# Performance work log

Measured on AMD Instinct MI355X. Metric: run time of the kernel, lower is better.

## Reference

```python
import jax, jax.numpy as jnp
import numpy as np

B, S, H = 2, 512, 768
E, M, R, R2 = 64, 64, 128, 128
NER_C, REL_C, SIZE_E, CLS = 10, 8, 32, 101
NEG = -1e30


def _linear(x, w, b):
    # torch nn.Linear convention: w is [out, in]
    return x @ w.T + b


def _span_pool(emb, masks):
    # emb [B,S,H], masks [B,K,S] -> masked max over tokens -> [B,K,H]
    neg = jnp.where(masks[..., None] != 0, 0.0, NEG)  # [B,K,S,1]
    return jnp.max(neg + emb[:, None, :, :], axis=2)


def _classify_spans(input_ids, emb, masks, size_emb, rep_w, rep_b, head_w, head_b):
    pool = _span_pool(emb, masks)                      # [B,K,H]
    cls_idx = jnp.argmax((input_ids == CLS).astype(jnp.int32), axis=1)
    ctx = emb[jnp.arange(emb.shape[0]), cls_idx]       # [B,H] (get_token)
    rep = jnp.concatenate([jnp.broadcast_to(ctx[:, None, :], pool.shape), pool, size_emb], axis=-1)
    clf = _linear(jax.nn.relu(_linear(rep, rep_w, rep_b)), head_w, head_b)
    return clf, pool


def _classify_relations(pool, size_emb, rels, rel_masks, emb, w1, b1, w2, b2, w3, b3):
    Bc = pool.shape[0]
    bidx = jnp.arange(Bc)[:, None, None]
    pairs = pool[bidx, rels].reshape(Bc, rels.shape[1], -1)        # [B,R,2H]
    size_pairs = size_emb[bidx, rels].reshape(Bc, rels.shape[1], -1)  # [B,R,2*SIZE_E]
    # masked max over context tokens (rel mask)
    ctx = jnp.max(jnp.where(rel_masks[..., None] != 0, 0.0, NEG) + emb[:, None, :, :], axis=2)
    ctx = jnp.where(jnp.any(rel_masks != 0, axis=-1)[..., None], ctx, 0.0)
    rel_repr = jnp.concatenate([ctx, pairs, size_pairs], axis=-1)  # [B,R,3H+2*SIZE_E]
    h = jax.nn.relu(_linear(rel_repr, w1, b1))
    h = jax.nn.relu(_linear(h, w2, b2))
    return _linear(h, w3, b3)


def setup_inputs():
    key = jax.random.key(0)
    ks = jax.random.split(key, 24)
    p = lambda k, shape: jax.random.normal(k, shape, jnp.float32) * 0.02
    ids = jax.random.randint(ks[0], (B, S), 2000, 30000)
    ids = ids.at[:, 0].set(CLS)  # exactly one cls token per row
    return dict(
        input_ids=ids,
        entity_masks=jax.random.randint(ks[1], (B, E, S), 0, 2).astype(jnp.int32),
        entity_sizes=jax.random.randint(ks[2], (B, E), 0, 100),
        mention_masks=jax.random.randint(ks[3], (B, M, S), 0, 2).astype(jnp.int32),
        mention_sizes=jax.random.randint(ks[4], (B, M), 0, 100),
        relations=jax.random.randint(ks[5], (B, R, 2), 0, E),
        rel_masks=jax.random.randint(ks[6], (B, R, S), 0, 2).astype(jnp.int32),
        references=jax.random.randint(ks[7], (B, R2, 2), 0, M),
        references_masks=jax.random.randint(ks[8], (B, R2, S), 0, 2).astype(jnp.int32),
        token_embedding=jax.random.normal(ks[9], (B, S, H), jnp.float32),
        ner_size_emb=p(ks[10], (100, SIZE_E)),
        emd_size_emb=p(ks[11], (100, SIZE_E)),
        ner_rep_w=p(ks[12], (H, 2 * H + SIZE_E)), ner_rep_b=jnp.zeros(H, jnp.float32),
        ner_head_w=p(ks[13], (NER_C, H)), ner_head_b=jnp.zeros(NER_C, jnp.float32),
        emd_rep_w=p(ks[14], (H, 2 * H + SIZE_E)), emd_rep_b=jnp.zeros(H, jnp.float32),
        emd_head_w=p(ks[15], (2, H)), emd_head_b=jnp.zeros(2, jnp.float32),
        rel_w1=p(ks[16], (H, 3 * H + 2 * SIZE_E)), rel_b1=jnp.zeros(H, jnp.float32),
        rel_w2=p(ks[17], (H, H)), rel_b2=jnp.zeros(H, jnp.float32),
        rel_w3=p(ks[18], (REL_C, H)), rel_b3=jnp.zeros(REL_C, jnp.float32),
        cr_w1=p(ks[19], (H, 3 * H + 2 * SIZE_E)), cr_b1=jnp.zeros(H, jnp.float32),
        cr_w2=p(ks[20], (H, H)), cr_b2=jnp.zeros(H, jnp.float32),
        cr_w3=p(ks[21], (1, H)), cr_b3=jnp.zeros(1, jnp.float32),
    )


def reference(input_ids, entity_masks, entity_sizes, mention_masks, mention_sizes,
              relations, rel_masks, references, references_masks, token_embedding,
              ner_size_emb, emd_size_emb,
              ner_rep_w, ner_rep_b, ner_head_w, ner_head_b,
              emd_rep_w, emd_rep_b, emd_head_w, emd_head_b,
              rel_w1, rel_b1, rel_w2, rel_b2, rel_w3, rel_b3,
              cr_w1, cr_b1, cr_w2, cr_b2, cr_w3, cr_b3):
    sz = ner_size_emb[entity_sizes]                                    # [B,E,SIZE_E]
    entity_clf, entity_pool = _classify_spans(input_ids, token_embedding, entity_masks, sz,
                                              ner_rep_w, ner_rep_b, ner_head_w, ner_head_b)
    rel_clf = _classify_relations(entity_pool, sz, relations, rel_masks, token_embedding,
                                  rel_w1, rel_b1, rel_w2, rel_b2, rel_w3, rel_b3)
    msz = emd_size_emb[mention_sizes]
    mention_clf, mention_pool = _classify_spans(input_ids, token_embedding, mention_masks, msz,
                                                emd_rep_w, emd_rep_b, emd_head_w, emd_head_b)
    ref_clf = _classify_relations(mention_pool, msz, references, references_masks, token_embedding,
                                  cr_w1, cr_b1, cr_w2, cr_b2, cr_w3, cr_b3)
    return entity_clf, rel_clf, mention_clf, ref_clf
```

## Files before the change

### kernel.cpp

```cpp
#include <hip/hip_runtime.h>
#include <hip/hip_bf16.h>

typedef __hip_bfloat16 bf16;
typedef __attribute__((ext_vector_type(8))) short short8;
typedef __attribute__((ext_vector_type(4))) float f32x4;

#define SS 512
#define HD 768
#define NEGC (-1e30f)
#define NSPLIT 8
#define TOK 64
#define POOL_BLOCKS 768
#define NCONV 128
#define D1_BLOCKS (POOL_BLOCKS + 4 + NCONV)

__device__ __forceinline__ short8 cvt8(float4 a, float4 b)
{
  union { bf16 h[8]; short8 s; } u;
  u.h[0] = __hip_bfloat16(a.x); u.h[1] = __hip_bfloat16(a.y);
  u.h[2] = __hip_bfloat16(a.z); u.h[3] = __hip_bfloat16(a.w);
  u.h[4] = __hip_bfloat16(b.x); u.h[5] = __hip_bfloat16(b.y);
  u.h[6] = __hip_bfloat16(b.z); u.h[7] = __hip_bfloat16(b.w);
  return u.s;
}

struct WC { const float* s; bf16* d; int n8; };
struct WC6 { WC c[6]; };

__global__ __launch_bounds__(256) void k_d1(
    const int* __restrict__ e_masks, const int* __restrict__ m_masks,
    const int* __restrict__ r_masks, const int* __restrict__ c_masks,
    const float* __restrict__ emb, const int* __restrict__ input_ids,
    const int* __restrict__ esizes, const int* __restrict__ msizes,
    const float* __restrict__ nsemb, const float* __restrict__ esemb,
    bf16* __restrict__ part, int* __restrict__ flags,
    bf16* __restrict__ sze, bf16* __restrict__ szm,
    bf16* __restrict__ ctxb, float* __restrict__ out, WC6 wc)
{
  int bx = blockIdx.x;
  int t  = threadIdx.x;

  if (bx >= POOL_BLOCKS) {
    int q = bx - POOL_BLOCKS;
    if (q == 0) {
      for (int i = t; i < 128 * 32; i += 256)
        sze[i] = __hip_bfloat16(nsemb[(size_t)esizes[i >> 5] * 32 + (i & 31)]);
    } else if (q == 1) {
      for (int i = t; i < 128 * 32; i += 256)
        szm[i] = __hip_bfloat16(esemb[(size_t)msizes[i >> 5] * 32 + (i & 31)]);
    } else if (q == 2) {
      __shared__ int s_cls;
      for (int b2 = 0; b2 < 2; b2++) {
        if (t == 0) s_cls = SS;
        __syncthreads();
        for (int s = t; s < SS; s += 256)
          if (input_ids[b2 * SS + s] == 101) atomicMin(&s_cls, s);
        __syncthreads();
        int ci = (s_cls == SS) ? 0 : s_cls;
        for (int hh = t; hh < HD; hh += 256)
          ctxb[(size_t)b2 * HD + hh] = __hip_bfloat16(emb[((size_t)b2 * SS + ci) * HD + hh]);
        __syncthreads();
      }
    } else if (q == 3) {
      for (int i = t; i < 3840; i += 256) out[i] = 0.f;
    } else {
      int cid = q - 4;
      #pragma unroll
      for (int seg = 0; seg < 6; seg++) {
        const float* s = wc.c[seg].s;
        bf16* dp = wc.c[seg].d;
        int n8 = wc.c[seg].n8;
        for (int i = cid * 256 + t; i < n8; i += NCONV * 256) {
          float4 f0 = *(const float4*)(s + (size_t)i * 8);
          float4 f1 = *(const float4*)(s + (size_t)i * 8 + 4);
          *(short8*)(dp + (size_t)i * 8) = cvt8(f0, f1);
        }
      }
    }
    return;
  }

  int g  = bx % 48;
  int b  = (bx / 48) & 1;
  int sp = bx / 96;
  int j0 = g * 8;

  const int* marr; int row0;
  if      (j0 < 64)  { marr = e_masks; row0 = b*64  +  j0;        }
  else if (j0 < 128) { marr = m_masks; row0 = b*64  + (j0-64);    }
  else if (j0 < 256) { marr = r_masks; row0 = b*128 + (j0-128);   }
  else               { marr = c_masks; row0 = b*128 + (j0-256);   }

  __shared__ unsigned s_pack[TOK];
  __shared__ unsigned s_any;
  if (t == 0) s_any = 0u;
  __syncthreads();

  int sbase = sp * TOK;
  if (t < TOK) {
    unsigned w = 0;
    #pragma unroll
    for (int k = 0; k < 8; k++) {
      int mm = marr[(size_t)(row0 + k) * SS + sbase + t];
      w |= (mm != 0 ? 1u : 0u) << k;
    }
    s_pack[t] = w;
    atomicOr(&s_any, w);
  }
  __syncthreads();

  float a0[8], a1[8], a2[8];
  #pragma unroll
  for (int k = 0; k < 8; k++) { a0[k] = -INFINITY; a1[k] = -INFINITY; a2[k] = -INFINITY; }

  const float* ep = emb + ((size_t)b * SS + sbase) * HD + t * 3;
  #pragma unroll 2
  for (int s = 0; s < TOK; s += 2) {
    float u0 = ep[0];
    float u1 = ep[1];
    float u2 = ep[2];
    float v0 = ep[HD];
    float v1 = ep[HD + 1];
    float v2 = ep[HD + 2];
    ep += 2 * HD;
    unsigned w0 = (unsigned)__builtin_amdgcn_readfirstlane((int)s_pack[s]);
    unsigned w1 = (unsigned)__builtin_amdgcn_readfirstlane((int)s_pack[s + 1]);
    #pragma unroll
    for (int k = 0; k < 8; k++) {
      float add0 = (w0 & (1u << k)) ? 0.f : NEGC;
      float add1 = (w1 & (1u << k)) ? 0.f : NEGC;
      a0[k] = fmaxf(fmaxf(a0[k], u0 + add0), v0 + add1);
      a1[k] = fmaxf(fmaxf(a1[k], u1 + add0), v1 + add1);
      a2[k] = fmaxf(fmaxf(a2[k], u2 + add0), v2 + add1);
    }
  }

  #pragma unroll
  for (int k = 0; k < 8; k++) {
    int sg = b * 384 + j0 + k;
    bf16* dst = part + ((size_t)sg * NSPLIT + sp) * HD + t * 3;
    dst[0] = __hip_bfloat16(a0[k]);
    dst[1] = __hip_bfloat16(a1[k]);
    dst[2] = __hip_bfloat16(a2[k]);
  }
  if (t < 8) flags[(size_t)(b * 384 + j0 + t) * NSPLIT + sp] = (int)((s_any >> t) & 1u);
}

__global__ __launch_bounds__(256) void k_combine(
    const bf16* __restrict__ part, const int* __restrict__ flags,
    bf16* __restrict__ epool, bf16* __restrict__ mpool,
    bf16* __restrict__ rctx, bf16* __restrict__ cctx)
{
  int sg = blockIdx.x;
  int b = sg / 384, j = sg % 384;
  int any = 0;
  #pragma unroll
  for (int sp = 0; sp < NSPLIT; sp++) any |= flags[(size_t)sg * NSPLIT + sp];

  int h = threadIdx.x * 3;
  float v0 = -INFINITY, v1 = -INFINITY, v2 = -INFINITY;
  #pragma unroll
  for (int sp = 0; sp < NSPLIT; sp++) {
    const bf16* src = part + ((size_t)sg * NSPLIT + sp) * HD + h;
    v0 = fmaxf(v0, (float)src[0]);
    v1 = fmaxf(v1, (float)src[1]);
    v2 = fmaxf(v2, (float)src[2]);
  }
  bf16* dst;
  if      (j < 64)  { dst = epool + ((size_t)b*64  + j)       * HD + h; }
  else if (j < 128) { dst = mpool + ((size_t)b*64  + (j-64))  * HD + h; }
  else if (j < 256) { dst = rctx  + ((size_t)b*128 + (j-128)) * HD + h;
                      if (!any) { v0 = 0.f; v1 = 0.f; v2 = 0.f; } }
  else              { dst = cctx  + ((size_t)b*128 + (j-256)) * HD + h;
                      if (!any) { v0 = 0.f; v1 = 0.f; v2 = 0.f; } }
  dst[0] = __hip_bfloat16(v0);
  dst[1] = __hip_bfloat16(v1);
  dst[2] = __hip_bfloat16(v2);
}

struct P1 {
  const bf16 *ctx, *pool, *sz; const int* ridx;
  const bf16* W; const float* bias;
  bf16* C;
  const float *hw, *hb; float* outp;
  int is_rel, N, K, Mtiles;
};
struct P1x4 { P1 p[4]; };

__global__ __launch_bounds__(256, 2) void k_gemm1(P1x4 args)
{
  int id = blockIdx.x;
  int x = id / 96;
  int r96 = id % 96;
  int y = r96 % 24, z = r96 / 24;
  P1 g = args.p[z];
  if (x >= g.Mtiles) return;
  int mt = x * 32, nt = y * 32;
  int wave = threadIdx.x >> 6, lane = threadIdx.x & 63;
  int lm = lane & 15, quad = lane >> 4;
  int K_ = g.K;

  const bf16 *g0[2], *g1[2], *g2[2], *g3[2], *g4[2];
  int rr[2] = { mt + lm, mt + 16 + lm };
  #pragma unroll
  for (int i = 0; i < 2; i++) {
    int rI = rr[i];
    if (g.is_rel) {
      int b = rI >> 7;
      int i0 = g.ridx[2 * rI], i1 = g.ridx[2 * rI + 1];
      g0[i] = g.ctx  + (size_t)rI * HD;
      g1[i] = g.pool + (size_t)(b * 64 + i0) * HD;
      g2[i] = g.pool + (size_t)(b * 64 + i1) * HD;
      g3[i] = g.sz   + (size_t)(b * 64 + i0) * 32;
      g4[i] = g.sz   + (size_t)(b * 64 + i1) * 32;
    } else {
      g0[i] = g.ctx  + (size_t)(rI >> 6) * HD;
      g1[i] = g.pool + (size_t)rI * HD;
      g2[i] = g.sz   + (size_t)rI * 32;
      g3[i] = g2[i]; g4[i] = g2[i];
    }
  }
  const bf16* w0p = g.W + (size_t)(nt + lm)      * K_ + quad * 8;
  const bf16* w1p = g.W + (size_t)(nt + 16 + lm) * K_ + quad * 8;

  f32x4 acc00 = {0.f,0.f,0.f,0.f}, acc01 = {0.f,0.f,0.f,0.f};
  f32x4 acc10 = {0.f,0.f,0.f,0.f}, acc11 = {0.f,0.f,0.f,0.f};

  for (int k32 = wave * 32; k32 < K_; k32 += 128) {
    const bf16 *b0, *b1;
    if      (k32 < 768)  { b0 = g0[0] + k32;          b1 = g0[1] + k32;          }
    else if (k32 < 1536) { b0 = g1[0] + (k32 - 768);  b1 = g1[1] + (k32 - 768);  }
    else if (k32 < 2304) { b0 = g2[0] + (k32 - 1536); b1 = g2[1] + (k32 - 1536); }
    else if (k32 < 2336) { b0 = g3[0] + (k32 - 2304); b1 = g3[1] + (k32 - 2304); }
    else                 { b0 = g4[0] + (k32 - 2336); b1 = g4[1] + (k32 - 2336); }
    short8 a0 = *(const short8*)((const short*)b0 + quad * 8);
    short8 a1 = *(const short8*)((const short*)b1 + quad * 8);
    short8 w0 = *(const short8*)(w0p + k32);
    short8 w1 = *(const short8*)(w1p + k32);
    acc00 = __builtin_amdgcn_mfma_f32_16x16x32_bf16(a0, w0, acc00, 0, 0, 0);
    acc01 = __builtin_amdgcn_mfma_f32_16x16x32_bf16(a0, w1, acc01, 0, 0, 0);
    acc10 = __builtin_amdgcn_mfma_f32_16x16x32_bf16(a1, w0, acc10, 0, 0, 0);
    acc11 = __builtin_amdgcn_mfma_f32_16x16x32_bf16(a1, w1, acc11, 0, 0, 0);
  }

  __shared__ float smem[4 * 32 * 32];
  #pragma unroll
  for (int reg = 0; reg < 4; reg++) {
    int rI = quad * 4 + reg;
    smem[wave*1024 + rI*32 + lm]             = acc00[reg];
    smem[wave*1024 + rI*32 + 16 + lm]        = acc01[reg];
    smem[wave*1024 + (16 + rI)*32 + lm]      = acc10[reg];
    smem[wave*1024 + (16 + rI)*32 + 16 + lm] = acc11[reg];
  }
  __syncthreads();

  int c = threadIdx.x & 31;
  int rb = threadIdx.x >> 5;
  float bb = g.bias[nt + c];
  #pragma unroll
  for (int i = 0; i < 4; i++) {
    int rI = rb + 8 * i;
    float v = smem[rI*32 + c] + smem[1024 + rI*32 + c] + smem[2048 + rI*32 + c] + smem[3072 + rI*32 + c];
    v = fmaxf(v + bb, 0.f);
    if (g.C) g.C[(size_t)(mt + rI) * HD + nt + c] = __hip_bfloat16(v);
    else     smem[rI*32 + c] = v;
  }
  __syncthreads();

  if (!g.C) {
    int rI = threadIdx.x >> 3, oi = threadIdx.x & 7;
    for (int o = oi; o < g.N; o += 8) {
      float s = 0.f;
      #pragma unroll
      for (int cc = 0; cc < 32; cc++) {
        int c2 = (cc + rI) & 31;
        s += smem[rI*32 + c2] * g.hw[(size_t)o * HD + nt + c2];
      }
      if (blockIdx.x % 96 < 24) ;
      if (y == 0) s += g.hb[o];
      atomicAdd(g.outp + (size_t)(mt + rI) * g.N + o, s);
    }
  }
}

struct P2 { const short* A; const bf16* W; const float* bias;
            const float *hw, *hb; float* outp; int N; };
struct P2x2 { P2 p[2]; };

__global__ __launch_bounds__(256, 2) void k_gemm2(P2x2 args)
{
  int id = blockIdx.x;
  int x = id / 48;
  int r48 = id % 48;
  int y = r48 % 24, z = r48 / 24;
  P2 g = args.p[z];
  int mt = x * 32, nt = y * 32;
  int wave = threadIdx.x >> 6, lane = threadIdx.x & 63;
  int lm = lane & 15, quad = lane >> 4;

  const short* a0p = g.A + (size_t)(mt + lm)      * HD + quad * 8;
  const short* a1p = g.A + (size_t)(mt + 16 + lm) * HD + quad * 8;
  const bf16* w0p = g.W + (size_t)(nt + lm)      * HD + quad * 8;
  const bf16* w1p = g.W + (size_t)(nt + 16 + lm) * HD + quad * 8;

  f32x4 acc00 = {0.f,0.f,0.f,0.f}, acc01 = {0.f,0.f,0.f,0.f};
  f32x4 acc10 = {0.f,0.f,0.f,0.f}, acc11 = {0.f,0.f,0.f,0.f};

  for (int k32 = wave * 32; k32 < HD; k32 += 128) {
    short8 a0 = *(const short8*)(a0p + k32);
    short8 a1 = *(const short8*)(a1p + k32);
    short8 w0 = *(const short8*)(w0p + k32);
    short8 w1 = *(const short8*)(w1p + k32);
    acc00 = __builtin_amdgcn_mfma_f32_16x16x32_bf16(a0, w0, acc00, 0, 0, 0);
    acc01 = __builtin_amdgcn_mfma_f32_16x16x32_bf16(a0, w1, acc01, 0, 0, 0);
    acc10 = __builtin_amdgcn_mfma_f32_16x16x32_bf16(a1, w0, acc10, 0, 0, 0);
    acc11 = __builtin_amdgcn_mfma_f32_16x16x32_bf16(a1, w1, acc11, 0, 0, 0);
  }

  __shared__ float smem[4 * 32 * 32];
  #pragma unroll
  for (int reg = 0; reg < 4; reg++) {
    int rI = quad * 4 + reg;
    smem[wave*1024 + rI*32 + lm]             = acc00[reg];
    smem[wave*1024 + rI*32 + 16 + lm]        = acc01[reg];
    smem[wave*1024 + (16 + rI)*32 + lm]      = acc10[reg];
    smem[wave*1024 + (16 + rI)*32 + 16 + lm] = acc11[reg];
  }
  __syncthreads();

  int c = threadIdx.x & 31;
  int rb = threadIdx.x >> 5;
  float bb = g.bias[nt + c];
  #pragma unroll
  for (int i = 0; i < 4; i++) {
    int rI = rb + 8 * i;
    float v = smem[rI*32 + c] + smem[1024 + rI*32 + c] + smem[2048 + rI*32 + c] + smem[3072 + rI*32 + c];
    smem[rI*32 + c] = fmaxf(v + bb, 0.f);
  }
  __syncthreads();

  int rI = threadIdx.x >> 3, oi = threadIdx.x & 7;
  for (int o = oi; o < g.N; o += 8) {
    float s = 0.f;
    #pragma unroll
    for (int cc = 0; cc < 32; cc++) {
      int c2 = (cc + rI) & 31;
      s += smem[rI*32 + c2] * g.hw[(size_t)o * HD + nt + c2];
    }
    if (y == 0) s += g.hb[o];
    atomicAdd(g.outp + (size_t)(mt + rI) * g.N + o, s);
  }
}

extern "C" void kernel_launch(void* const* d_in, const int* in_sizes, int n_in,
                              void* d_out, int out_size, void* d_ws, size_t ws_size,
                              hipStream_t stream)
{
  const int*   input_ids  = (const int*)d_in[0];
  const int*   e_masks    = (const int*)d_in[1];
  const int*   e_sizes    = (const int*)d_in[2];
  const int*   m_masks    = (const int*)d_in[3];
  const int*   m_sizes    = (const int*)d_in[4];
  const int*   relations  = (const int*)d_in[5];
  const int*   r_masks    = (const int*)d_in[6];
  const int*   references = (const int*)d_in[7];
  const int*   c_masks    = (const int*)d_in[8];
  const float* emb        = (const float*)d_in[9];
  const float* nsemb      = (const float*)d_in[10];
  const float* esemb      = (const float*)d_in[11];
  const float* ner_rep_w  = (const float*)d_in[12];
  const float* ner_rep_b  = (const float*)d_in[13];
  const float* ner_head_w = (const float*)d_in[14];
  const float* ner_head_b = (const float*)d_in[15];
  const float* emd_rep_w  = (const float*)d_in[16];
  const float* emd_rep_b  = (const float*)d_in[17];
  const float* emd_head_w = (const float*)d_in[18];
  const float* emd_head_b = (const float*)d_in[19];
  const float* rel_w1 = (const float*)d_in[20];
  const float* rel_b1 = (const float*)d_in[21];
  const float* rel_w2 = (const float*)d_in[22];
  const float* rel_b2 = (const float*)d_in[23];
  const float* rel_w3 = (const float*)d_in[24];
  const float* rel_b3 = (const float*)d_in[25];
  const float* cr_w1 = (const float*)d_in[26];
  const float* cr_b1 = (const float*)d_in[27];
  const float* cr_w2 = (const float*)d_in[28];
  const float* cr_b2 = (const float*)d_in[29];
  const float* cr_w3 = (const float*)d_in[30];
  const float* cr_b3 = (const float*)d_in[31];
  float* out = (float*)d_out;

  bf16* wsb = (bf16*)d_ws;
  size_t ob = 0;
  bf16* PART  = wsb + ob; ob += (size_t)NSPLIT * 768 * HD;
  bf16* EPOOL = wsb + ob; ob += (size_t)128 * HD;
  bf16* MPOOL = wsb + ob; ob += (size_t)128 * HD;
  bf16* RCTX  = wsb + ob; ob += (size_t)256 * HD;
  bf16* CCTX  = wsb + ob; ob += (size_t)256 * HD;
  bf16* SZE   = wsb + ob; ob += (size_t)128 * 32;
  bf16* SZM   = wsb + ob; ob += (size_t)128 * 32;
  bf16* CTXB  = wsb + ob; ob += (size_t)2 * HD;
  bf16* RH1   = wsb + ob; ob += (size_t)256 * HD;
  bf16* CH1   = wsb + ob; ob += (size_t)256 * HD;
  int*  FLAGS = (int*)(wsb + ob); ob += (size_t)2 * NSPLIT * 768;
  bf16* WB_NER = wsb + ob; ob += (size_t)HD * 1568;
  bf16* WB_EMD = wsb + ob; ob += (size_t)HD * 1568;
  bf16* WB_RW1 = wsb + ob; ob += (size_t)HD * 2368;
  bf16* WB_CW1 = wsb + ob; ob += (size_t)HD * 2368;
  bf16* WB_RW2 = wsb + ob; ob += (size_t)HD * HD;
  bf16* WB_CW2 = wsb + ob; ob += (size_t)HD * HD;

  WC6 wc;
  wc.c[0] = { ner_rep_w, WB_NER, HD * 1568 / 8 };
  wc.c[1] = { emd_rep_w, WB_EMD, HD * 1568 / 8 };
  wc.c[2] = { rel_w1,    WB_RW1, HD * 2368 / 8 };
  wc.c[3] = { cr_w1,     WB_CW1, HD * 2368 / 8 };
  wc.c[4] = { rel_w2,    WB_RW2, HD * HD / 8 };
  wc.c[5] = { cr_w2,     WB_CW2, HD * HD / 8 };

  k_d1<<<D1_BLOCKS, 256, 0, stream>>>(
      e_masks, m_masks, r_masks, c_masks, emb, input_ids,
      e_sizes, m_sizes, nsemb, esemb,
      PART, FLAGS, SZE, SZM, CTXB, out, wc);

  k_combine<<<768, 256, 0, stream>>>(PART, FLAGS, EPOOL, MPOOL, RCTX, CCTX);

  P1x4 a1;
  a1.p[0] = { CTXB, EPOOL, SZE, nullptr,    WB_NER, ner_rep_b,
              nullptr, ner_head_w, ner_head_b, out,        0, 10, 1568, 4 };
  a1.p[1] = { CTXB, MPOOL, SZM, nullptr,    WB_EMD, emd_rep_b,
              nullptr, emd_head_w, emd_head_b, out + 3328, 0, 2,  1568, 4 };
  a1.p[2] = { RCTX, EPOOL, SZE, relations,  WB_RW1, rel_b1,
              RH1, nullptr, nullptr, nullptr,              1, 0,  2368, 8 };
  a1.p[3] = { CCTX, MPOOL, SZM, references, WB_CW1, cr_b1,
              CH1, nullptr, nullptr, nullptr,              1, 0,  2368, 8 };
  k_gemm1<<<8 * 96, 256, 0, stream>>>(a1);

  P2x2 a2;
  a2.p[0] = { (const short*)RH1, WB_RW2, rel_b2, rel_w3, rel_b3, out + 1280, 8 };
  a2.p[1] = { (const short*)CH1, WB_CW2, cr_b2,  cr_w3,  cr_b3,  out + 3584, 1 };
  k_gemm2<<<8 * 48, 256, 0, stream>>>(a2);
}
```

Measured before the change: 190.7 us.

## Pool 16 spans per block, prefetch GEMM operands, compact GEMM grids

The pooling kernel now processes 16 spans per block instead of 8, halving the block count so each embedding load is reused across more masks. The cost is 48 accumulator registers per thread. Both GEMM kernels gain software prefetching of the next K-slice operands, so global loads overlap the MFMA work. The gemm1 grid is remapped to launch only the valid tiles, removing the early-exit blocks, and gemm2's block decomposition is reordered.

Measured after the change: 201.0 us. 5.4% more time.

```diff
diff --git a/kernel.cpp b/kernel.cpp
--- a/kernel.cpp
+++ b/kernel.cpp
@@ -10,7 +10,8 @@
 #define NEGC (-1e30f)
 #define NSPLIT 8
 #define TOK 64
-#define POOL_BLOCKS 768
+#define NSPAN 16
+#define POOL_BLOCKS 384
 #define NCONV 128
 #define D1_BLOCKS (POOL_BLOCKS + 4 + NCONV)
 
@@ -80,10 +81,10 @@
     return;
   }
 
-  int g  = bx % 48;
-  int b  = (bx / 48) & 1;
-  int sp = bx / 96;
-  int j0 = g * 8;
+  int g  = bx % 24;
+  int b  = (bx / 24) & 1;
+  int sp = bx / 48;
+  int j0 = g * NSPAN;
 
   const int* marr; int row0;
   if      (j0 < 64)  { marr = e_masks; row0 = b*64  +  j0;        }
@@ -100,7 +101,7 @@
   if (t < TOK) {
     unsigned w = 0;
     #pragma unroll
-    for (int k = 0; k < 8; k++) {
+    for (int k = 0; k < NSPAN; k++) {
       int mm = marr[(size_t)(row0 + k) * SS + sbase + t];
       w |= (mm != 0 ? 1u : 0u) << k;
     }
@@ -109,12 +110,11 @@
   }
   __syncthreads();
 
-  float a0[8], a1[8], a2[8];
-  #pragma unroll
-  for (int k = 0; k < 8; k++) { a0[k] = -INFINITY; a1[k] = -INFINITY; a2[k] = -INFINITY; }
+  float a0[NSPAN], a1[NSPAN], a2[NSPAN];
+  #pragma unroll
+  for (int k = 0; k < NSPAN; k++) { a0[k] = -INFINITY; a1[k] = -INFINITY; a2[k] = -INFINITY; }
 
   const float* ep = emb + ((size_t)b * SS + sbase) * HD + t * 3;
-  #pragma unroll 2
   for (int s = 0; s < TOK; s += 2) {
     float u0 = ep[0];
     float u1 = ep[1];
@@ -126,7 +126,7 @@
     unsigned w0 = (unsigned)__builtin_amdgcn_readfirstlane((int)s_pack[s]);
     unsigned w1 = (unsigned)__builtin_amdgcn_readfirstlane((int)s_pack[s + 1]);
     #pragma unroll
-    for (int k = 0; k < 8; k++) {
+    for (int k = 0; k < NSPAN; k++) {
       float add0 = (w0 & (1u << k)) ? 0.f : NEGC;
       float add1 = (w1 & (1u << k)) ? 0.f : NEGC;
       a0[k] = fmaxf(fmaxf(a0[k], u0 + add0), v0 + add1);
@@ -136,14 +136,14 @@
   }
 
   #pragma unroll
-  for (int k = 0; k < 8; k++) {
+  for (int k = 0; k < NSPAN; k++) {
     int sg = b * 384 + j0 + k;
     bf16* dst = part + ((size_t)sg * NSPLIT + sp) * HD + t * 3;
     dst[0] = __hip_bfloat16(a0[k]);
     dst[1] = __hip_bfloat16(a1[k]);
     dst[2] = __hip_bfloat16(a2[k]);
   }
-  if (t < 8) flags[(size_t)(b * 384 + j0 + t) * NSPLIT + sp] = (int)((s_any >> t) & 1u);
+  if (t < NSPAN) flags[(size_t)(b * 384 + j0 + t) * NSPLIT + sp] = (int)((s_any >> t) & 1u);
 }
 
 __global__ __launch_bounds__(256) void k_combine(
@@ -190,11 +190,13 @@
 __global__ __launch_bounds__(256, 2) void k_gemm1(P1x4 args)
 {
   int id = blockIdx.x;
-  int x = id / 96;
-  int r96 = id % 96;
-  int y = r96 % 24, z = r96 / 24;
+  int z, rem;
+  if      (id < 96)  { z = 0; rem = id;       }
+  else if (id < 192) { z = 1; rem = id - 96;  }
+  else if (id < 384) { z = 2; rem = id - 192; }
+  else               { z = 3; rem = id - 384; }
+  int x = rem / 24, y = rem % 24;
   P1 g = args.p[z];
-  if (x >= g.Mtiles) return;
   int mt = x * 32, nt = y * 32;
   int wave = threadIdx.x >> 6, lane = threadIdx.x & 63;
   int lm = lane & 15, quad = lane >> 4;
@@ -226,22 +228,37 @@
   f32x4 acc00 = {0.f,0.f,0.f,0.f}, acc01 = {0.f,0.f,0.f,0.f};
   f32x4 acc10 = {0.f,0.f,0.f,0.f}, acc11 = {0.f,0.f,0.f,0.f};
 
-  for (int k32 = wave * 32; k32 < K_; k32 += 128) {
+  auto ldA = [&](int k32, short8& a0, short8& a1) {
     const bf16 *b0, *b1;
     if      (k32 < 768)  { b0 = g0[0] + k32;          b1 = g0[1] + k32;          }
     else if (k32 < 1536) { b0 = g1[0] + (k32 - 768);  b1 = g1[1] + (k32 - 768);  }
     else if (k32 < 2304) { b0 = g2[0] + (k32 - 1536); b1 = g2[1] + (k32 - 1536); }
     else if (k32 < 2336) { b0 = g3[0] + (k32 - 2304); b1 = g3[1] + (k32 - 2304); }
     else                 { b0 = g4[0] + (k32 - 2336); b1 = g4[1] + (k32 - 2336); }
-    short8 a0 = *(const short8*)((const short*)b0 + quad * 8);
-    short8 a1 = *(const short8*)((const short*)b1 + quad * 8);
-    short8 w0 = *(const short8*)(w0p + k32);
-    short8 w1 = *(const short8*)(w1p + k32);
+    a0 = *(const short8*)((const short*)b0 + quad * 8);
+    a1 = *(const short8*)((const short*)b1 + quad * 8);
+  };
+
+  int k32 = wave * 32;
+  short8 a0, a1, w0, w1;
+  ldA(k32, a0, a1);
+  w0 = *(const short8*)(w0p + k32);
+  w1 = *(const short8*)(w1p + k32);
+  for (int kn = k32 + 128; kn < K_; kn += 128) {
+    short8 na0, na1, nw0, nw1;
+    ldA(kn, na0, na1);
+    nw0 = *(const short8*)(w0p + kn);
+    nw1 = *(const short8*)(w1p + kn);
     acc00 = __builtin_amdgcn_mfma_f32_16x16x32_bf16(a0, w0, acc00, 0, 0, 0);
     acc01 = __builtin_amdgcn_mfma_f32_16x16x32_bf16(a0, w1, acc01, 0, 0, 0);
     acc10 = __builtin_amdgcn_mfma_f32_16x16x32_bf16(a1, w0, acc10, 0, 0, 0);
     acc11 = __builtin_amdgcn_mfma_f32_16x16x32_bf16(a1, w1, acc11, 0, 0, 0);
-  }
+    a0 = na0; a1 = na1; w0 = nw0; w1 = nw1;
+  }
+  acc00 = __builtin_amdgcn_mfma_f32_16x16x32_bf16(a0, w0, acc00, 0, 0, 0);
+  acc01 = __builtin_amdgcn_mfma_f32_16x16x32_bf16(a0, w1, acc01, 0, 0, 0);
+  acc10 = __builtin_amdgcn_mfma_f32_16x16x32_bf16(a1, w0, acc10, 0, 0, 0);
+  acc11 = __builtin_amdgcn_mfma_f32_16x16x32_bf16(a1, w1, acc11, 0, 0, 0);
 
   __shared__ float smem[4 * 32 * 32];
   #pragma unroll
@@ -276,7 +293,6 @@
         int c2 = (cc + rI) & 31;
         s += smem[rI*32 + c2] * g.hw[(size_t)o * HD + nt + c2];
       }
-      if (blockIdx.x % 96 < 24) ;
       if (y == 0) s += g.hb[o];
       atomicAdd(g.outp + (size_t)(mt + rI) * g.N + o, s);
     }
@@ -290,9 +306,9 @@
 __global__ __launch_bounds__(256, 2) void k_gemm2(P2x2 args)
 {
   int id = blockIdx.x;
-  int x = id / 48;
-  int r48 = id % 48;
-  int y = r48 % 24, z = r48 / 24;
+  int z = id / 192;
+  int rem = id % 192;
+  int x = rem / 24, y = rem % 24;
   P2 g = args.p[z];
   int mt = x * 32, nt = y * 32;
   int wave = threadIdx.x >> 6, lane = threadIdx.x & 63;
@@ -306,16 +322,26 @@
   f32x4 acc00 = {0.f,0.f,0.f,0.f}, acc01 = {0.f,0.f,0.f,0.f};
   f32x4 acc10 = {0.f,0.f,0.f,0.f}, acc11 = {0.f,0.f,0.f,0.f};
 
-  for (int k32 = wave * 32; k32 < HD; k32 += 128) {
-    short8 a0 = *(const short8*)(a0p + k32);
-    short8 a1 = *(const short8*)(a1p + k32);
-    short8 w0 = *(const short8*)(w0p + k32);
-    short8 w1 = *(const short8*)(w1p + k32);
+  int k32 = wave * 32;
+  short8 a0 = *(const short8*)(a0p + k32);
+  short8 a1 = *(const short8*)(a1p + k32);
+  short8 w0 = *(const short8*)(w0p + k32);
+  short8 w1 = *(const short8*)(w1p + k32);
+  for (int kn = k32 + 128; kn < HD; kn += 128) {
+    short8 na0 = *(const short8*)(a0p + kn);
+    short8 na1 = *(const short8*)(a1p + kn);
+    short8 nw0 = *(const short8*)(w0p + kn);
+    short8 nw1 = *(const short8*)(w1p + kn);
     acc00 = __builtin_amdgcn_mfma_f32_16x16x32_bf16(a0, w0, acc00, 0, 0, 0);
     acc01 = __builtin_amdgcn_mfma_f32_16x16x32_bf16(a0, w1, acc01, 0, 0, 0);
     acc10 = __builtin_amdgcn_mfma_f32_16x16x32_bf16(a1, w0, acc10, 0, 0, 0);
     acc11 = __builtin_amdgcn_mfma_f32_16x16x32_bf16(a1, w1, acc11, 0, 0, 0);
-  }
+    a0 = na0; a1 = na1; w0 = nw0; w1 = nw1;
+  }
+  acc00 = __builtin_amdgcn_mfma_f32_16x16x32_bf16(a0, w0, acc00, 0, 0, 0);
+  acc01 = __builtin_amdgcn_mfma_f32_16x16x32_bf16(a0, w1, acc01, 0, 0, 0);
+  acc10 = __builtin_amdgcn_mfma_f32_16x16x32_bf16(a1, w0, acc10, 0, 0, 0);
+  acc11 = __builtin_amdgcn_mfma_f32_16x16x32_bf16(a1, w1, acc11, 0, 0, 0);
 
   __shared__ float smem[4 * 32 * 32];
   #pragma unroll
@@ -434,10 +460,10 @@
               RH1, nullptr, nullptr, nullptr,              1, 0,  2368, 8 };
   a1.p[3] = { CCTX, MPOOL, SZM, references, WB_CW1, cr_b1,
               CH1, nullptr, nullptr, nullptr,              1, 0,  2368, 8 };
-  k_gemm1<<<8 * 96, 256, 0, stream>>>(a1);
+  k_gemm1<<<576, 256, 0, stream>>>(a1);
 
   P2x2 a2;
   a2.p[0] = { (const short*)RH1, WB_RW2, rel_b2, rel_w3, rel_b3, out + 1280, 8 };
   a2.p[1] = { (const short*)CH1, WB_CW2, cr_b2,  cr_w3,  cr_b3,  out + 3584, 1 };
-  k_gemm2<<<8 * 48, 256, 0, stream>>>(a2);
-}
+  k_gemm2<<<384, 256, 0, stream>>>(a2);
+}
```

## Pre-tile bf16 weights and hidden activations into MFMA fragment layout

Applied to the files above, without the earlier changes.

The fp32-to-bf16 weight conversion now writes the weights in a 16-row by 32-column fragment-blocked layout, so each MFMA operand load in the GEMMs reads a contiguous 512-element tile instead of striding across rows. The first GEMM writes its hidden output in the same tiled layout for the second GEMM to consume. Conversion work is split into per-16-row units over more blocks. The first GEMM grid is compacted so it no longer launches idle blocks for the entity and mention tasks. This trades a more complex index mapping in conversion and epilogue for better-coalesced weight and activation reads.

Measured after the change: 187.2 us. Within noise of the previous version (-1.8%).

```diff
diff --git a/kernel.cpp b/kernel.cpp
--- a/kernel.cpp
+++ b/kernel.cpp
@@ -11,7 +11,7 @@
 #define NSPLIT 8
 #define TOK 64
 #define POOL_BLOCKS 768
-#define NCONV 128
+#define NCONV 252
 #define D1_BLOCKS (POOL_BLOCKS + 4 + NCONV)
 
 __device__ __forceinline__ short8 cvt8(float4 a, float4 b)
@@ -24,7 +24,7 @@
   return u.s;
 }
 
-struct WC { const float* s; bf16* d; int n8; };
+struct WC { const float* s; bf16* d; int K; };
 struct WC6 { WC c[6]; };
 
 __global__ __launch_bounds__(256) void k_d1(
@@ -65,15 +65,23 @@
       for (int i = t; i < 3840; i += 256) out[i] = 0.f;
     } else {
       int cid = q - 4;
-      #pragma unroll
-      for (int seg = 0; seg < 6; seg++) {
+      for (int u = cid; u < 288; u += NCONV) {
+        int seg = u / 48, nblk = u % 48;
         const float* s = wc.c[seg].s;
         bf16* dp = wc.c[seg].d;
-        int n8 = wc.c[seg].n8;
-        for (int i = cid * 256 + t; i < n8; i += NCONV * 256) {
-          float4 f0 = *(const float4*)(s + (size_t)i * 8);
-          float4 f1 = *(const float4*)(s + (size_t)i * 8 + 4);
-          *(short8*)(dp + (size_t)i * 8) = cvt8(f0, f1);
+        int K = wc.c[seg].K;
+        int KB = K >> 5;
+        int nchunk = K * 2;
+        const float* srow = s + (size_t)nblk * 16 * K;
+        bf16* drow = dp + (size_t)nblk * KB * 512;
+        for (int c8 = t; c8 < nchunk; c8 += 256) {
+          int kblk = c8 >> 6;
+          int lm   = (c8 >> 2) & 15;
+          int quad = c8 & 3;
+          const float* sp = srow + (size_t)lm * K + kblk * 32 + quad * 8;
+          float4 f0 = *(const float4*)sp;
+          float4 f1 = *(const float4*)(sp + 4);
+          *(short8*)(drow + (size_t)kblk * 512 + lm * 32 + quad * 8) = cvt8(f0, f1);
         }
       }
     }
@@ -190,15 +198,18 @@
 __global__ __launch_bounds__(256, 2) void k_gemm1(P1x4 args)
 {
   int id = blockIdx.x;
-  int x = id / 96;
-  int r96 = id % 96;
-  int y = r96 % 24, z = r96 / 24;
+  int z, rem;
+  if      (id < 96)  { z = 0; rem = id;       }
+  else if (id < 192) { z = 1; rem = id - 96;  }
+  else if (id < 384) { z = 2; rem = id - 192; }
+  else               { z = 3; rem = id - 384; }
+  int x = rem / 24, y = rem % 24;
   P1 g = args.p[z];
-  if (x >= g.Mtiles) return;
   int mt = x * 32, nt = y * 32;
   int wave = threadIdx.x >> 6, lane = threadIdx.x & 63;
   int lm = lane & 15, quad = lane >> 4;
   int K_ = g.K;
+  int KB = K_ >> 5;
 
   const bf16 *g0[2], *g1[2], *g2[2], *g3[2], *g4[2];
   int rr[2] = { mt + lm, mt + 16 + lm };
@@ -220,8 +231,8 @@
       g3[i] = g2[i]; g4[i] = g2[i];
     }
   }
-  const bf16* w0p = g.W + (size_t)(nt + lm)      * K_ + quad * 8;
-  const bf16* w1p = g.W + (size_t)(nt + 16 + lm) * K_ + quad * 8;
+  const bf16* w0p = g.W + (size_t)(nt >> 4) * KB * 512 + lm * 32 + quad * 8;
+  const bf16* w1p = w0p + (size_t)KB * 512;
 
   f32x4 acc00 = {0.f,0.f,0.f,0.f}, acc01 = {0.f,0.f,0.f,0.f};
   f32x4 acc10 = {0.f,0.f,0.f,0.f}, acc11 = {0.f,0.f,0.f,0.f};
@@ -235,8 +246,8 @@
     else                 { b0 = g4[0] + (k32 - 2336); b1 = g4[1] + (k32 - 2336); }
     short8 a0 = *(const short8*)((const short*)b0 + quad * 8);
     short8 a1 = *(const short8*)((const short*)b1 + quad * 8);
-    short8 w0 = *(const short8*)(w0p + k32);
-    short8 w1 = *(const short8*)(w1p + k32);
+    short8 w0 = *(const short8*)(w0p + (size_t)k32 * 16);
+    short8 w1 = *(const short8*)(w1p + (size_t)k32 * 16);
     acc00 = __builtin_amdgcn_mfma_f32_16x16x32_bf16(a0, w0, acc00, 0, 0, 0);
     acc01 = __builtin_amdgcn_mfma_f32_16x16x32_bf16(a0, w1, acc01, 0, 0, 0);
     acc10 = __builtin_amdgcn_mfma_f32_16x16x32_bf16(a1, w0, acc10, 0, 0, 0);
@@ -262,8 +273,13 @@
     int rI = rb + 8 * i;
     float v = smem[rI*32 + c] + smem[1024 + rI*32 + c] + smem[2048 + rI*32 + c] + smem[3072 + rI*32 + c];
     v = fmaxf(v + bb, 0.f);
-    if (g.C) g.C[(size_t)(mt + rI) * HD + nt + c] = __hip_bfloat16(v);
-    else     smem[rI*32 + c] = v;
+    if (g.C) {
+      size_t off = ((size_t)((mt >> 4) + (rI >> 4)) * 24 + (nt >> 5)) * 512
+                 + (size_t)(rI & 15) * 32 + (c >> 3) * 8 + (c & 7);
+      g.C[off] = __hip_bfloat16(v);
+    } else {
+      smem[rI*32 + c] = v;
+    }
   }
   __syncthreads();
 
@@ -276,14 +292,13 @@
         int c2 = (cc + rI) & 31;
         s += smem[rI*32 + c2] * g.hw[(size_t)o * HD + nt + c2];
       }
-      if (blockIdx.x % 96 < 24) ;
       if (y == 0) s += g.hb[o];
       atomicAdd(g.outp + (size_t)(mt + rI) * g.N + o, s);
     }
   }
 }
 
-struct P2 { const short* A; const bf16* W; const float* bias;
+struct P2 { const bf16* A; const bf16* W; const float* bias;
             const float *hw, *hb; float* outp; int N; };
 struct P2x2 { P2 p[2]; };
 
@@ -298,19 +313,20 @@
   int wave = threadIdx.x >> 6, lane = threadIdx.x & 63;
   int lm = lane & 15, quad = lane >> 4;
 
-  const short* a0p = g.A + (size_t)(mt + lm)      * HD + quad * 8;
-  const short* a1p = g.A + (size_t)(mt + 16 + lm) * HD + quad * 8;
-  const bf16* w0p = g.W + (size_t)(nt + lm)      * HD + quad * 8;
-  const bf16* w1p = g.W + (size_t)(nt + 16 + lm) * HD + quad * 8;
+  const bf16* a0p = g.A + (size_t)(mt >> 4) * 24 * 512 + lm * 32 + quad * 8;
+  const bf16* a1p = a0p + 24 * 512;
+  const bf16* w0p = g.W + (size_t)(nt >> 4) * 24 * 512 + lm * 32 + quad * 8;
+  const bf16* w1p = w0p + 24 * 512;
 
   f32x4 acc00 = {0.f,0.f,0.f,0.f}, acc01 = {0.f,0.f,0.f,0.f};
   f32x4 acc10 = {0.f,0.f,0.f,0.f}, acc11 = {0.f,0.f,0.f,0.f};
 
   for (int k32 = wave * 32; k32 < HD; k32 += 128) {
-    short8 a0 = *(const short8*)(a0p + k32);
-    short8 a1 = *(const short8*)(a1p + k32);
-    short8 w0 = *(const short8*)(w0p + k32);
-    short8 w1 = *(const short8*)(w1p + k32);
+    size_t fo = (size_t)k32 * 16;
+    short8 a0 = *(const short8*)(a0p + fo);
+    short8 a1 = *(const short8*)(a1p + fo);
+    short8 w0 = *(const short8*)(w0p + fo);
+    short8 w1 = *(const short8*)(w1p + fo);
     acc00 = __builtin_amdgcn_mfma_f32_16x16x32_bf16(a0, w0, acc00, 0, 0, 0);
     acc01 = __builtin_amdgcn_mfma_f32_16x16x32_bf16(a0, w1, acc01, 0, 0, 0);
     acc10 = __builtin_amdgcn_mfma_f32_16x16x32_bf16(a1, w0, acc10, 0, 0, 0);
@@ -411,12 +427,12 @@
   bf16* WB_CW2 = wsb + ob; ob += (size_t)HD * HD;
 
   WC6 wc;
-  wc.c[0] = { ner_rep_w, WB_NER, HD * 1568 / 8 };
-  wc.c[1] = { emd_rep_w, WB_EMD, HD * 1568 / 8 };
-  wc.c[2] = { rel_w1,    WB_RW1, HD * 2368 / 8 };
-  wc.c[3] = { cr_w1,     WB_CW1, HD * 2368 / 8 };
-  wc.c[4] = { rel_w2,    WB_RW2, HD * HD / 8 };
-  wc.c[5] = { cr_w2,     WB_CW2, HD * HD / 8 };
+  wc.c[0] = { ner_rep_w, WB_NER, 1568 };
+  wc.c[1] = { emd_rep_w, WB_EMD, 1568 };
+  wc.c[2] = { rel_w1,    WB_RW1, 2368 };
+  wc.c[3] = { cr_w1,     WB_CW1, 2368 };
+  wc.c[4] = { rel_w2,    WB_RW2, 768 };
+  wc.c[5] = { cr_w2,     WB_CW2, 768 };
 
   k_d1<<<D1_BLOCKS, 256, 0, stream>>>(
       e_masks, m_masks, r_masks, c_masks, emb, input_ids,
@@ -434,10 +450,10 @@
               RH1, nullptr, nullptr, nullptr,              1, 0,  2368, 8 };
   a1.p[3] = { CCTX, MPOOL, SZM, references, WB_CW1, cr_b1,
               CH1, nullptr, nullptr, nullptr,              1, 0,  2368, 8 };
-  k_gemm1<<<8 * 96, 256, 0, stream>>>(a1);
+  k_gemm1<<<576, 256, 0, stream>>>(a1);
 
   P2x2 a2;
-  a2.p[0] = { (const short*)RH1, WB_RW2, rel_b2, rel_w3, rel_b3, out + 1280, 8 };
-  a2.p[1] = { (const short*)CH1, WB_CW2, cr_b2,  cr_w3,  cr_b3,  out + 3584, 1 };
-  k_gemm2<<<8 * 48, 256, 0, stream>>>(a2);
-}
+  a2.p[0] = { RH1, WB_RW2, rel_b2, rel_w3, rel_b3, out + 1280, 8 };
+  a2.p[1] = { CH1, WB_CW2, cr_b2,  cr_w3,  cr_b3,  out + 3584, 1 };
+  k_gemm2<<<384, 256, 0, stream>>>(a2);
+}
```
